# Optimization experiments

Measured on AMD Instinct MI355X. Metric: run time of the kernel, lower is better.

Reference implementation:

```python
import jax, jax.numpy as jnp
import numpy as np

B, N, DIN, DOUT = 8, 2048, 512, 512
EDGE_P = 0.01  # edge probability for the random binary adjacency


def setup_inputs() -> dict:
    key = jax.random.key(0)
    k1, k2, k3, k4 = jax.random.split(key, 4)
    inputs = jax.random.normal(k1, (B, N, DIN), dtype=jnp.float32)
    # binary dense adjacency (dense_to_sparse discards weights -> edges are adj != 0)
    adj = (jax.random.uniform(k2, (B, N, N)) < EDGE_P).astype(jnp.float32)
    W = jax.random.normal(k3, (DIN, DOUT), dtype=jnp.float32) / np.sqrt(DIN)
    b = jax.random.normal(k4, (DOUT,), dtype=jnp.float32) * 0.01
    return {"inputs": inputs, "adj": adj, "W": W, "b": b}


def _gcn_norm(adj):
    # binary edge mask (edge weights from dense_to_sparse are discarded)
    A = (adj != 0).astype(adj.dtype)
    # add remaining self-loops: force diagonal to 1
    eye = jnp.eye(A.shape[-1], dtype=A.dtype)
    A = jnp.maximum(A, eye)
    deg = A.sum(axis=-1)                       # [B, N]
    dinv = jnp.where(deg > 0, jax.lax.rsqrt(deg), 0.0)
    # D^-1/2 (A + I) D^-1/2
    return dinv[..., :, None] * A * dinv[..., None, :]


def reference(inputs, adj, W, b):
    norm = _gcn_norm(adj)                      # [B, N, N]
    h = jnp.einsum('bnf,fo->bno', inputs, W)   # linear (no internal bias)
    agg = jnp.einsum('bnm,bmo->bno', norm, h)  # degree-normalized aggregation
    return jnp.tanh(agg + b)
```

## Files before the change

kernel.cpp:

```cpp
#include <hip/hip_runtime.h>
#include <hip/hip_bf16.h>
#include <math.h>


#define NROWS 16384
#define NCOLS 2048
#define DF    512
#define CAP   64

typedef __attribute__((ext_vector_type(8))) short bf16x8;
typedef __attribute__((ext_vector_type(4))) float f32x4;
typedef const void __attribute__((address_space(1))) gvoid_t;
typedef void __attribute__((address_space(3))) svoid_t;

__global__ __launch_bounds__(256) void scan_wt(
    const float* __restrict__ W, __hip_bfloat16* __restrict__ WT,
    const float* __restrict__ adj, int* __restrict__ cnt,
    int* __restrict__ edges, float* __restrict__ dinv) {
  __shared__ float t[64][65];
  const int blk = blockIdx.x;
  const int tid = threadIdx.x;
  if (blk < 64) {
    const int bx = blk & 7, by = blk >> 3;
    const int tx = tid & 63, ty = tid >> 6;
    #pragma unroll
    for (int i = 0; i < 16; ++i)
      t[ty + i * 4][tx] = W[(size_t)(by * 64 + ty + i * 4) * DF + bx * 64 + tx];
    __syncthreads();
    #pragma unroll
    for (int i = 0; i < 16; ++i)
      WT[(size_t)(bx * 64 + ty + i * 4) * DF + by * 64 + tx] =
          __float2bfloat16(t[tx][ty + i * 4]);
    return;
  }
  const int lane = tid & 63;
  const int wv = tid >> 6;
  const int rbase = (blk - 64) * 16 + wv * 4;
  float4 cur[8], nxt[8];
  {
    const float4* r4 = (const float4*)(adj + (size_t)rbase * NCOLS);
    #pragma unroll
    for (int k = 0; k < 8; ++k) cur[k] = r4[k * 64 + lane];
  }
  #pragma unroll
  for (int g = 0; g < 4; ++g) {
    const int r = rbase + g;
    if (g < 3) {
      const float4* rn = (const float4*)(adj + (size_t)(r + 1) * NCOLS);
      #pragma unroll
      for (int k = 0; k < 8; ++k) nxt[k] = rn[k * 64 + lane];
    }
    const int n = r & (NCOLS - 1);
    unsigned m = 0;
    #pragma unroll
    for (int k = 0; k < 8; ++k) {
      m |= (cur[k].x != 0.0f ? 1u : 0u) << (4 * k);
      m |= (cur[k].y != 0.0f ? 1u : 0u) << (4 * k + 1);
      m |= (cur[k].z != 0.0f ? 1u : 0u) << (4 * k + 2);
      m |= (cur[k].w != 0.0f ? 1u : 0u) << (4 * k + 3);
    }
    if (lane == ((n >> 2) & 63))
      m |= 1u << (((n >> 8) << 2) | (n & 3));
    const int c_ = __popc(m);
    int inc = c_;
    #pragma unroll
    for (int off = 1; off < 64; off <<= 1) {
      const int tv = __shfl_up(inc, off);
      if (lane >= off) inc += tv;
    }
    const int tot = __shfl(inc, 63);
    int p = inc - c_;
    unsigned mm = m;
    const size_t eb = (size_t)r * CAP;
    while (mm) {
      const int bpos = __ffs(mm) - 1;
      mm &= mm - 1;
      if (p < CAP)
        edges[eb + p] = ((bpos >> 2) << 8) + (lane << 2) + (bpos & 3);
      ++p;
    }
    if (lane == 63) {
      cnt[r] = tot < CAP ? tot : CAP;
      dinv[r] = rsqrtf((float)tot);
    }
    #pragma unroll
    for (int k = 0; k < 8; ++k) cur[k] = nxt[k];
  }
}

__global__ __launch_bounds__(256) void gemm_k(
    const float* __restrict__ X, const __hip_bfloat16* __restrict__ WT,
    __hip_bfloat16* __restrict__ H) {
  __shared__ __hip_bfloat16 As[2][64 * 32];
  __shared__ __hip_bfloat16 Bs[2][128 * 32];
  const int tid = threadIdx.x;
  const int lane = tid & 63;
  const int w = tid >> 6;
  const int id = blockIdx.x;
  const int xcd = id & 7;
  const int q = id >> 3;
  const int bm = (xcd * 32 + (q >> 2)) * 64;
  const int bn = (q & 3) * 128;

  const int wm = (w >> 1) * 32;
  const int wn = (w & 1) * 64;
  const int srow = tid >> 2;
  const int scol = (tid & 3) * 8;
  const int kl = (lane >> 4) * 8;
  const int rl = lane & 15;

  f32x4 acc[2][4] = {};
  float4 ar0, ar1;

  #define LOAD_A(k0)  do {                                              \
    const float4* g_ = (const float4*)(X + (size_t)(bm + srow) * DF + (k0) + scol); \
    ar0 = g_[0]; ar1 = g_[1]; } while (0)

  #define STAGE_B(k0, buf)  do {                                        \
    _Pragma("unroll")                                                   \
    for (int i = 0; i < 2; ++i) {                                       \
      const __hip_bfloat16* gb = WT + (size_t)(bn + i * 64 + srow) * DF + (k0) + scol; \
      char* lb = (char*)&Bs[buf][0] + i * 4096 + w * 1024;              \
      __builtin_amdgcn_global_load_lds((gvoid_t*)gb, (svoid_t*)lb, 16, 0, 0); \
    } } while (0)

  #define WRITE_A(buf)  do {                                            \
    float xs[8];                                                        \
    *(float4*)&xs[0] = ar0; *(float4*)&xs[4] = ar1;                     \
    union { __hip_bfloat16 hh[8]; uint4 q_; } pk;                       \
    _Pragma("unroll")                                                   \
    for (int i = 0; i < 8; ++i) pk.hh[i] = __float2bfloat16(xs[i]);     \
    char* la = (char*)&As[buf][0] + srow * 64 + scol * 2;               \
    *(uint4*)la = pk.q_; } while (0)

  LOAD_A(0);
  STAGE_B(0, 0);
  WRITE_A(0);
  __syncthreads();

  for (int t = 0; t < 16; ++t) {
    const int c_ = t & 1, nx = c_ ^ 1;
    if (t < 15) {
      LOAD_A((t + 1) * 32);
      STAGE_B((t + 1) * 32, nx);
    }
    bf16x8 af[2], bf[4];
    #pragma unroll
    for (int mi = 0; mi < 2; ++mi)
      af[mi] = *(const bf16x8*)&As[c_][(wm + mi * 16 + rl) * 32 + kl];
    #pragma unroll
    for (int ni = 0; ni < 4; ++ni)
      bf[ni] = *(const bf16x8*)&Bs[c_][(wn + ni * 16 + rl) * 32 + kl];
    #pragma unroll
    for (int mi = 0; mi < 2; ++mi)
      #pragma unroll
      for (int ni = 0; ni < 4; ++ni)
        acc[mi][ni] = __builtin_amdgcn_mfma_f32_16x16x32_bf16(af[mi], bf[ni], acc[mi][ni], 0, 0, 0);
    if (t < 15) WRITE_A(nx);
    __syncthreads();
  }

  const int rq = (lane >> 4) * 4;
  #pragma unroll
  for (int mi = 0; mi < 2; ++mi)
    #pragma unroll
    for (int ni = 0; ni < 4; ++ni) {
      const int col = bn + wn + ni * 16 + rl;
      #pragma unroll
      for (int j = 0; j < 4; ++j) {
        const int row = bm + wm + mi * 16 + rq + j;
        H[(size_t)row * DF + col] = __float2bfloat16(acc[mi][ni][j]);
      }
    }
  #undef LOAD_A
  #undef STAGE_B
  #undef WRITE_A
}

__device__ __forceinline__ float fast_tanh(float x) {
  const float t = __expf(2.0f * x);
  return 1.0f - __fdividef(2.0f, t + 1.0f);
}

__global__ __launch_bounds__(256) void aggregate(
    const __hip_bfloat16* __restrict__ h, const int* __restrict__ cnt,
    const int* __restrict__ edges, const float* __restrict__ dinv,
    const float* __restrict__ bias, float* __restrict__ out) {
  const int lane = threadIdx.x & 63;
  const int wv = threadIdx.x >> 6;
  const int batch = blockIdx.x & 7;
  const int qb = blockIdx.x >> 3;
  const int rn = qb * 4 + wv;
  const int r = (batch << 11) + rn;
  const int c = cnt[r];
  const float* dv = dinv + (batch << 11);
  const uint4* hbase = (const uint4*)(h + (size_t)(batch << 11) * DF);
  const int* eb = edges + (size_t)r * CAP;

  float acc[8] = {0.f,0.f,0.f,0.f,0.f,0.f,0.f,0.f};
  for (int e = 0; e < c; e += 8) {
    int   mj[8];
    float wj[8];
    uint4 vj[8];
    #pragma unroll
    for (int j = 0; j < 8; ++j)
      if (e + j < c) mj[j] = eb[e + j];
    #pragma unroll
    for (int j = 0; j < 8; ++j)
      if (e + j < c) {
        wj[j] = dv[mj[j]];
        vj[j] = hbase[(size_t)mj[j] * 64 + lane];
      }
    #pragma unroll
    for (int j = 0; j < 8; ++j)
      if (e + j < c) {
        const float wt = wj[j];
        acc[0] += wt * __uint_as_float(vj[j].x << 16);
        acc[1] += wt * __uint_as_float(vj[j].x & 0xffff0000u);
        acc[2] += wt * __uint_as_float(vj[j].y << 16);
        acc[3] += wt * __uint_as_float(vj[j].y & 0xffff0000u);
        acc[4] += wt * __uint_as_float(vj[j].z << 16);
        acc[5] += wt * __uint_as_float(vj[j].z & 0xffff0000u);
        acc[6] += wt * __uint_as_float(vj[j].w << 16);
        acc[7] += wt * __uint_as_float(vj[j].w & 0xffff0000u);
      }
  }
  const float4* b4 = (const float4*)bias;
  const float4 bb0 = b4[lane * 2];
  const float4 bb1 = b4[lane * 2 + 1];
  const float dn = dv[rn];
  float4 o;
  float* op = out + (size_t)r * DF + lane * 8;
  o.x = fast_tanh(acc[0] * dn + bb0.x);
  o.y = fast_tanh(acc[1] * dn + bb0.y);
  o.z = fast_tanh(acc[2] * dn + bb0.z);
  o.w = fast_tanh(acc[3] * dn + bb0.w);
  *(float4*)op = o;
  o.x = fast_tanh(acc[4] * dn + bb1.x);
  o.y = fast_tanh(acc[5] * dn + bb1.y);
  o.z = fast_tanh(acc[6] * dn + bb1.z);
  o.w = fast_tanh(acc[7] * dn + bb1.w);
  *(float4*)(op + 4) = o;
}

extern "C" void kernel_launch(void* const* d_in, const int* in_sizes, int n_in,
                              void* d_out, int out_size, void* d_ws, size_t ws_size,
                              hipStream_t stream) {
  const float* X    = (const float*)d_in[0];
  const float* adj  = (const float*)d_in[1];
  const float* W    = (const float*)d_in[2];
  const float* bias = (const float*)d_in[3];
  float* out = (float*)d_out;

  char* ws = (char*)d_ws;
  __hip_bfloat16* h    = (__hip_bfloat16*)(ws);
  __hip_bfloat16* WT   = (__hip_bfloat16*)(ws + 16777216);
  float*          dinv = (float*)(ws + 17301504);
  int*            cnt  = (int*)  (ws + 17367040);
  int*            edges= (int*)  (ws + 17432576);

  scan_wt<<<1088, 256, 0, stream>>>(W, WT, adj, cnt, edges, dinv);
  gemm_k<<<1024, 256, 0, stream>>>(X, WT, h);
  aggregate<<<4096, 256, 0, stream>>>(h, cnt, edges, dinv, bias, out);
}
```

Before: 70.34 us.

## Split each row's edge list across four waves with LDS reduction in aggregate

The aggregate kernel now assigns one output row per block instead of one per wave. The four waves each process a quarter of the row's edges and combine their partial sums through shared memory. This shortens each wave's serial gather chain (about 21 edges per row on average) and launches four times as many blocks to expose more memory-level parallelism. In exchange it adds a __syncthreads, LDS traffic and a narrower float2 output store, and each wave's loop now covers only a few edges, so the unrolled batch of eight is mostly masked.

```diff
diff --git a/kernel.cpp b/kernel.cpp
--- a/kernel.cpp
+++ b/kernel.cpp
@@ -186,34 +186,38 @@
     const __hip_bfloat16* __restrict__ h, const int* __restrict__ cnt,
     const int* __restrict__ edges, const float* __restrict__ dinv,
     const float* __restrict__ bias, float* __restrict__ out) {
+  __shared__ float red[4][64][9];
   const int lane = threadIdx.x & 63;
   const int wv = threadIdx.x >> 6;
   const int batch = blockIdx.x & 7;
-  const int qb = blockIdx.x >> 3;
-  const int rn = qb * 4 + wv;
+  const int rn = blockIdx.x >> 3;
   const int r = (batch << 11) + rn;
   const int c = cnt[r];
   const float* dv = dinv + (batch << 11);
   const uint4* hbase = (const uint4*)(h + (size_t)(batch << 11) * DF);
   const int* eb = edges + (size_t)r * CAP;
 
+  const int quarter = (c + 3) >> 2;
+  const int e0 = wv * quarter;
+  const int e1 = min(e0 + quarter, c);
+
   float acc[8] = {0.f,0.f,0.f,0.f,0.f,0.f,0.f,0.f};
-  for (int e = 0; e < c; e += 8) {
+  for (int e = e0; e < e1; e += 8) {
     int   mj[8];
     float wj[8];
     uint4 vj[8];
     #pragma unroll
     for (int j = 0; j < 8; ++j)
-      if (e + j < c) mj[j] = eb[e + j];
+      if (e + j < e1) mj[j] = eb[e + j];
     #pragma unroll
     for (int j = 0; j < 8; ++j)
-      if (e + j < c) {
+      if (e + j < e1) {
         wj[j] = dv[mj[j]];
         vj[j] = hbase[(size_t)mj[j] * 64 + lane];
       }
     #pragma unroll
     for (int j = 0; j < 8; ++j)
-      if (e + j < c) {
+      if (e + j < e1) {
         const float wt = wj[j];
         acc[0] += wt * __uint_as_float(vj[j].x << 16);
         acc[1] += wt * __uint_as_float(vj[j].x & 0xffff0000u);
@@ -225,22 +229,22 @@
         acc[7] += wt * __uint_as_float(vj[j].w & 0xffff0000u);
       }
   }
-  const float4* b4 = (const float4*)bias;
-  const float4 bb0 = b4[lane * 2];
-  const float4 bb1 = b4[lane * 2 + 1];
+  #pragma unroll
+  for (int j = 0; j < 8; ++j) red[wv][lane][j] = acc[j];
+  __syncthreads();
+
+  const int f = wv * 128 + lane * 2;
+  const int l2 = f >> 3;
+  const int j2 = f & 7;
+  const float s0 = red[0][l2][j2]     + red[1][l2][j2]
+                 + red[2][l2][j2]     + red[3][l2][j2];
+  const float s1 = red[0][l2][j2 + 1] + red[1][l2][j2 + 1]
+                 + red[2][l2][j2 + 1] + red[3][l2][j2 + 1];
   const float dn = dv[rn];
-  float4 o;
-  float* op = out + (size_t)r * DF + lane * 8;
-  o.x = fast_tanh(acc[0] * dn + bb0.x);
-  o.y = fast_tanh(acc[1] * dn + bb0.y);
-  o.z = fast_tanh(acc[2] * dn + bb0.z);
-  o.w = fast_tanh(acc[3] * dn + bb0.w);
-  *(float4*)op = o;
-  o.x = fast_tanh(acc[4] * dn + bb1.x);
-  o.y = fast_tanh(acc[5] * dn + bb1.y);
-  o.z = fast_tanh(acc[6] * dn + bb1.z);
-  o.w = fast_tanh(acc[7] * dn + bb1.w);
-  *(float4*)(op + 4) = o;
+  float2 o;
+  o.x = fast_tanh(s0 * dn + bias[f]);
+  o.y = fast_tanh(s1 * dn + bias[f + 1]);
+  *(float2*)(out + (size_t)r * DF + f) = o;
 }
 
 extern "C" void kernel_launch(void* const* d_in, const int* in_sizes, int n_in,
@@ -261,5 +265,5 @@
 
   scan_wt<<<1088, 256, 0, stream>>>(W, WT, adj, cnt, edges, dinv);
   gemm_k<<<1024, 256, 0, stream>>>(X, WT, h);
-  aggregate<<<4096, 256, 0, stream>>>(h, cnt, edges, dinv, bias, out);
-}
+  aggregate<<<NROWS, 256, 0, stream>>>(h, cnt, edges, dinv, bias, out);
+}
```

Measured after the change: 73.08 us. 1.04x slower.

## Split W transpose into own kernel and co-schedule adjacency scan with GEMM

Applied to the files above, without the earlier changes.

The W transpose moves into a small standalone kernel, and the adjacency scan now shares one launch with the X·W GEMM: blocks 0-1023 run the GEMM and blocks 1024+ scan adjacency rows. The aim is to overlap the bandwidth-bound 128MB adjacency read with the compute-bound GEMM and to remove one kernel boundary. The scan also drops its double-buffered next-row registers and reloads into cur after building the mask, which lowers register use. The cost is that scan blocks now carry the GEMM's LDS allocation, which can limit occupancy, and the scan gets less load-latency hiding.

```diff
diff --git a/kernel.cpp b/kernel.cpp
--- a/kernel.cpp
+++ b/kernel.cpp
@@ -13,168 +13,164 @@
 typedef const void __attribute__((address_space(1))) gvoid_t;
 typedef void __attribute__((address_space(3))) svoid_t;
 
-__global__ __launch_bounds__(256) void scan_wt(
-    const float* __restrict__ W, __hip_bfloat16* __restrict__ WT,
-    const float* __restrict__ adj, int* __restrict__ cnt,
-    int* __restrict__ edges, float* __restrict__ dinv) {
+__global__ __launch_bounds__(256) void wt_kernel(
+    const float* __restrict__ W, __hip_bfloat16* __restrict__ WT) {
   __shared__ float t[64][65];
-  const int blk = blockIdx.x;
+  const int b2 = blockIdx.x;
+  const int bx = b2 & 7, by = b2 >> 3;
   const int tid = threadIdx.x;
-  if (blk < 64) {
-    const int bx = blk & 7, by = blk >> 3;
-    const int tx = tid & 63, ty = tid >> 6;
-    #pragma unroll
-    for (int i = 0; i < 16; ++i)
-      t[ty + i * 4][tx] = W[(size_t)(by * 64 + ty + i * 4) * DF + bx * 64 + tx];
-    __syncthreads();
-    #pragma unroll
-    for (int i = 0; i < 16; ++i)
-      WT[(size_t)(bx * 64 + ty + i * 4) * DF + by * 64 + tx] =
-          __float2bfloat16(t[tx][ty + i * 4]);
-    return;
-  }
+  const int tx = tid & 63, ty = tid >> 6;
+  #pragma unroll
+  for (int i = 0; i < 16; ++i)
+    t[ty + i * 4][tx] = W[(size_t)(by * 64 + ty + i * 4) * DF + bx * 64 + tx];
+  __syncthreads();
+  #pragma unroll
+  for (int i = 0; i < 16; ++i)
+    WT[(size_t)(bx * 64 + ty + i * 4) * DF + by * 64 + tx] =
+        __float2bfloat16(t[tx][ty + i * 4]);
+}
+
+__global__ __launch_bounds__(256) void fused_k(
+    const float* __restrict__ X, const __hip_bfloat16* __restrict__ WT,
+    const float* __restrict__ adj, __hip_bfloat16* __restrict__ H,
+    int* __restrict__ cnt, int* __restrict__ edges, float* __restrict__ dinv) {
+  __shared__ __hip_bfloat16 As[2][64 * 32];
+  __shared__ __hip_bfloat16 Bs[2][128 * 32];
+  const int id = blockIdx.x;
+  const int tid = threadIdx.x;
   const int lane = tid & 63;
   const int wv = tid >> 6;
-  const int rbase = (blk - 64) * 16 + wv * 4;
-  float4 cur[8], nxt[8];
-  {
-    const float4* r4 = (const float4*)(adj + (size_t)rbase * NCOLS);
-    #pragma unroll
-    for (int k = 0; k < 8; ++k) cur[k] = r4[k * 64 + lane];
+
+  if (id < 1024) {
+    const int xcd = id & 7;
+    const int q = id >> 3;
+    const int bm = (xcd * 32 + (q >> 2)) * 64;
+    const int bn = (q & 3) * 128;
+    const int w = wv;
+    const int wm = (w >> 1) * 32;
+    const int wn = (w & 1) * 64;
+    const int srow = tid >> 2;
+    const int scol = (tid & 3) * 8;
+    const int kl = (lane >> 4) * 8;
+    const int rl = lane & 15;
+
+    f32x4 acc[2][4] = {};
+    float4 ar0, ar1;
+
+    #define LOAD_A(k0)  do {                                              \
+      const float4* g_ = (const float4*)(X + (size_t)(bm + srow) * DF + (k0) + scol); \
+      ar0 = g_[0]; ar1 = g_[1]; } while (0)
+
+    #define STAGE_B(k0, buf)  do {                                        \
+      _Pragma("unroll")                                                   \
+      for (int i = 0; i < 2; ++i) {                                       \
+        const __hip_bfloat16* gb = WT + (size_t)(bn + i * 64 + srow) * DF + (k0) + scol; \
+        char* lb = (char*)&Bs[buf][0] + i * 4096 + w * 1024;              \
+        __builtin_amdgcn_global_load_lds((gvoid_t*)gb, (svoid_t*)lb, 16, 0, 0); \
+      } } while (0)
+
+    #define WRITE_A(buf)  do {                                            \
+      float xs[8];                                                        \
+      *(float4*)&xs[0] = ar0; *(float4*)&xs[4] = ar1;                     \
+      union { __hip_bfloat16 hh[8]; uint4 q_; } pk;                       \
+      _Pragma("unroll")                                                   \
+      for (int i = 0; i < 8; ++i) pk.hh[i] = __float2bfloat16(xs[i]);     \
+      char* la = (char*)&As[buf][0] + srow * 64 + scol * 2;               \
+      *(uint4*)la = pk.q_; } while (0)
+
+    LOAD_A(0);
+    STAGE_B(0, 0);
+    WRITE_A(0);
+    __syncthreads();
+
+    for (int t = 0; t < 16; ++t) {
+      const int c_ = t & 1, nx = c_ ^ 1;
+      if (t < 15) {
+        LOAD_A((t + 1) * 32);
+        STAGE_B((t + 1) * 32, nx);
+      }
+      bf16x8 af[2], bf[4];
+      #pragma unroll
+      for (int mi = 0; mi < 2; ++mi)
+        af[mi] = *(const bf16x8*)&As[c_][(wm + mi * 16 + rl) * 32 + kl];
+      #pragma unroll
+      for (int ni = 0; ni < 4; ++ni)
+        bf[ni] = *(const bf16x8*)&Bs[c_][(wn + ni * 16 + rl) * 32 + kl];
+      #pragma unroll
+      for (int mi = 0; mi < 2; ++mi)
+        #pragma unroll
+        for (int ni = 0; ni < 4; ++ni)
+          acc[mi][ni] = __builtin_amdgcn_mfma_f32_16x16x32_bf16(af[mi], bf[ni], acc[mi][ni], 0, 0, 0);
+      if (t < 15) WRITE_A(nx);
+      __syncthreads();
+    }
+
+    const int rq = (lane >> 4) * 4;
+    #pragma unroll
+    for (int mi = 0; mi < 2; ++mi)
+      #pragma unroll
+      for (int ni = 0; ni < 4; ++ni) {
+        const int col = bn + wn + ni * 16 + rl;
+        #pragma unroll
+        for (int j = 0; j < 4; ++j) {
+          const int row = bm + wm + mi * 16 + rq + j;
+          H[(size_t)row * DF + col] = __float2bfloat16(acc[mi][ni][j]);
+        }
+      }
+    #undef LOAD_A
+    #undef STAGE_B
+    #undef WRITE_A
+  } else {
+    const int rbase = (id - 1024) * 16 + wv * 4;
+    float4 cur[8];
+    {
+      const float4* r4 = (const float4*)(adj + (size_t)rbase * NCOLS);
+      #pragma unroll
+      for (int k = 0; k < 8; ++k) cur[k] = r4[k * 64 + lane];
+    }
+    #pragma unroll
+    for (int g = 0; g < 4; ++g) {
+      const int r = rbase + g;
+      const int n = r & (NCOLS - 1);
+      unsigned m = 0;
+      #pragma unroll
+      for (int k = 0; k < 8; ++k) {
+        m |= (cur[k].x != 0.0f ? 1u : 0u) << (4 * k);
+        m |= (cur[k].y != 0.0f ? 1u : 0u) << (4 * k + 1);
+        m |= (cur[k].z != 0.0f ? 1u : 0u) << (4 * k + 2);
+        m |= (cur[k].w != 0.0f ? 1u : 0u) << (4 * k + 3);
+      }
+      if (g < 3) {
+        const float4* rn = (const float4*)(adj + (size_t)(r + 1) * NCOLS);
+        #pragma unroll
+        for (int k = 0; k < 8; ++k) cur[k] = rn[k * 64 + lane];
+      }
+      if (lane == ((n >> 2) & 63))
+        m |= 1u << (((n >> 8) << 2) | (n & 3));
+      const int c_ = __popc(m);
+      int inc = c_;
+      #pragma unroll
+      for (int off = 1; off < 64; off <<= 1) {
+        const int tv = __shfl_up(inc, off);
+        if (lane >= off) inc += tv;
+      }
+      const int tot = __shfl(inc, 63);
+      int p = inc - c_;
+      unsigned mm = m;
+      const size_t eb = (size_t)r * CAP;
+      while (mm) {
+        const int bpos = __ffs(mm) - 1;
+        mm &= mm - 1;
+        if (p < CAP)
+          edges[eb + p] = ((bpos >> 2) << 8) + (lane << 2) + (bpos & 3);
+        ++p;
+      }
+      if (lane == 63) {
+        cnt[r] = tot < CAP ? tot : CAP;
+        dinv[r] = rsqrtf((float)tot);
+      }
+    }
   }
-  #pragma unroll
-  for (int g = 0; g < 4; ++g) {
-    const int r = rbase + g;
-    if (g < 3) {
-      const float4* rn = (const float4*)(adj + (size_t)(r + 1) * NCOLS);
-      #pragma unroll
-      for (int k = 0; k < 8; ++k) nxt[k] = rn[k * 64 + lane];
-    }
-    const int n = r & (NCOLS - 1);
-    unsigned m = 0;
-    #pragma unroll
-    for (int k = 0; k < 8; ++k) {
-      m |= (cur[k].x != 0.0f ? 1u : 0u) << (4 * k);
-      m |= (cur[k].y != 0.0f ? 1u : 0u) << (4 * k + 1);
-      m |= (cur[k].z != 0.0f ? 1u : 0u) << (4 * k + 2);
-      m |= (cur[k].w != 0.0f ? 1u : 0u) << (4 * k + 3);
-    }
-    if (lane == ((n >> 2) & 63))
-      m |= 1u << (((n >> 8) << 2) | (n & 3));
-    const int c_ = __popc(m);
-    int inc = c_;
-    #pragma unroll
-    for (int off = 1; off < 64; off <<= 1) {
-      const int tv = __shfl_up(inc, off);
-      if (lane >= off) inc += tv;
-    }
-    const int tot = __shfl(inc, 63);
-    int p = inc - c_;
-    unsigned mm = m;
-    const size_t eb = (size_t)r * CAP;
-    while (mm) {
-      const int bpos = __ffs(mm) - 1;
-      mm &= mm - 1;
-      if (p < CAP)
-        edges[eb + p] = ((bpos >> 2) << 8) + (lane << 2) + (bpos & 3);
-      ++p;
-    }
-    if (lane == 63) {
-      cnt[r] = tot < CAP ? tot : CAP;
-      dinv[r] = rsqrtf((float)tot);
-    }
-    #pragma unroll
-    for (int k = 0; k < 8; ++k) cur[k] = nxt[k];
-  }
-}
-
-__global__ __launch_bounds__(256) void gemm_k(
-    const float* __restrict__ X, const __hip_bfloat16* __restrict__ WT,
-    __hip_bfloat16* __restrict__ H) {
-  __shared__ __hip_bfloat16 As[2][64 * 32];
-  __shared__ __hip_bfloat16 Bs[2][128 * 32];
-  const int tid = threadIdx.x;
-  const int lane = tid & 63;
-  const int w = tid >> 6;
-  const int id = blockIdx.x;
-  const int xcd = id & 7;
-  const int q = id >> 3;
-  const int bm = (xcd * 32 + (q >> 2)) * 64;
-  const int bn = (q & 3) * 128;
-
-  const int wm = (w >> 1) * 32;
-  const int wn = (w & 1) * 64;
-  const int srow = tid >> 2;
-  const int scol = (tid & 3) * 8;
-  const int kl = (lane >> 4) * 8;
-  const int rl = lane & 15;
-
-  f32x4 acc[2][4] = {};
-  float4 ar0, ar1;
-
-  #define LOAD_A(k0)  do {                                              \
-    const float4* g_ = (const float4*)(X + (size_t)(bm + srow) * DF + (k0) + scol); \
-    ar0 = g_[0]; ar1 = g_[1]; } while (0)
-
-  #define STAGE_B(k0, buf)  do {                                        \
-    _Pragma("unroll")                                                   \
-    for (int i = 0; i < 2; ++i) {                                       \
-      const __hip_bfloat16* gb = WT + (size_t)(bn + i * 64 + srow) * DF + (k0) + scol; \
-      char* lb = (char*)&Bs[buf][0] + i * 4096 + w * 1024;              \
-      __builtin_amdgcn_global_load_lds((gvoid_t*)gb, (svoid_t*)lb, 16, 0, 0); \
-    } } while (0)
-
-  #define WRITE_A(buf)  do {                                            \
-    float xs[8];                                                        \
-    *(float4*)&xs[0] = ar0; *(float4*)&xs[4] = ar1;                     \
-    union { __hip_bfloat16 hh[8]; uint4 q_; } pk;                       \
-    _Pragma("unroll")                                                   \
-    for (int i = 0; i < 8; ++i) pk.hh[i] = __float2bfloat16(xs[i]);     \
-    char* la = (char*)&As[buf][0] + srow * 64 + scol * 2;               \
-    *(uint4*)la = pk.q_; } while (0)
-
-  LOAD_A(0);
-  STAGE_B(0, 0);
-  WRITE_A(0);
-  __syncthreads();
-
-  for (int t = 0; t < 16; ++t) {
-    const int c_ = t & 1, nx = c_ ^ 1;
-    if (t < 15) {
-      LOAD_A((t + 1) * 32);
-      STAGE_B((t + 1) * 32, nx);
-    }
-    bf16x8 af[2], bf[4];
-    #pragma unroll
-    for (int mi = 0; mi < 2; ++mi)
-      af[mi] = *(const bf16x8*)&As[c_][(wm + mi * 16 + rl) * 32 + kl];
-    #pragma unroll
-    for (int ni = 0; ni < 4; ++ni)
-      bf[ni] = *(const bf16x8*)&Bs[c_][(wn + ni * 16 + rl) * 32 + kl];
-    #pragma unroll
-    for (int mi = 0; mi < 2; ++mi)
-      #pragma unroll
-      for (int ni = 0; ni < 4; ++ni)
-        acc[mi][ni] = __builtin_amdgcn_mfma_f32_16x16x32_bf16(af[mi], bf[ni], acc[mi][ni], 0, 0, 0);
-    if (t < 15) WRITE_A(nx);
-    __syncthreads();
-  }
-
-  const int rq = (lane >> 4) * 4;
-  #pragma unroll
-  for (int mi = 0; mi < 2; ++mi)
-    #pragma unroll
-    for (int ni = 0; ni < 4; ++ni) {
-      const int col = bn + wn + ni * 16 + rl;
-      #pragma unroll
-      for (int j = 0; j < 4; ++j) {
-        const int row = bm + wm + mi * 16 + rq + j;
-        H[(size_t)row * DF + col] = __float2bfloat16(acc[mi][ni][j]);
-      }
-    }
-  #undef LOAD_A
-  #undef STAGE_B
-  #undef WRITE_A
 }
 
 __device__ __forceinline__ float fast_tanh(float x) {
@@ -259,7 +255,7 @@
   int*            cnt  = (int*)  (ws + 17367040);
   int*            edges= (int*)  (ws + 17432576);
 
-  scan_wt<<<1088, 256, 0, stream>>>(W, WT, adj, cnt, edges, dinv);
-  gemm_k<<<1024, 256, 0, stream>>>(X, WT, h);
+  wt_kernel<<<64, 256, 0, stream>>>(W, WT);
+  fused_k<<<2048, 256, 0, stream>>>(X, WT, adj, h, cnt, edges, dinv);
   aggregate<<<4096, 256, 0, stream>>>(h, cnt, edges, dinv, bias, out);
 }
```

Result: slower. 72.25 us (+2.7%).
